# Optimization experiments

Measured on AMD Instinct MI355X. Metric: run time of the kernel, lower is better.

## Reference

```python
import jax, jax.numpy as jnp
import numpy as np

B, S, V, D = 64, 24, 50257, 300
N, E, Ln, Le = 256, 1024, 4, 4
HL = 512               # LSTM hidden size
HEADS, HD = 4, 128
OUT = HEADS * HD       # 512, GAT out dim (concat heads)
NA = 3000              # num answers


def setup_inputs() -> dict:
    key = jax.random.key(0)
    ks = jax.random.split(key, 24)
    s = 0.02
    inp = {}
    inp["question"] = jax.random.randint(ks[0], (B, S), 0, V)
    inp["question_mask"] = jnp.ones((B, S), dtype=jnp.int32)
    inp["node_tokens"] = jax.random.randint(ks[1], (B, N, Ln), 0, V)
    inp["edge_tokens"] = jax.random.randint(ks[2], (B, E, Le), 0, V)
    inp["src_ids"] = jax.random.randint(ks[3], (B, E), 0, N)
    inp["dst_ids"] = jax.random.randint(ks[4], (B, E), 0, N)
    inp["word_emb"] = jax.random.normal(ks[5], (V, D)) * s
    inp["W_ih"] = jax.random.normal(ks[6], (D, 4 * HL)) * s
    inp["W_hh"] = jax.random.normal(ks[7], (HL, 4 * HL)) * s
    inp["b_lstm"] = jnp.zeros((4 * HL,))
    inp["W_node"] = jax.random.normal(ks[8], (D, HEADS * HD)) * s
    inp["W_rel"] = jax.random.normal(ks[9], (D, HEADS * HD)) * s
    inp["a_src"] = jax.random.normal(ks[10], (HEADS, HD)) * s
    inp["a_dst"] = jax.random.normal(ks[11], (HEADS, HD)) * s
    inp["a_edge"] = jax.random.normal(ks[12], (HEADS, HD)) * s
    inp["W_edge_upd"] = jax.random.normal(ks[13], (D, D)) * s
    inp["W_qnode"] = jax.random.normal(ks[14], (HL, OUT)) * s
    inp["b_qnode"] = jnp.zeros((OUT,))
    inp["W_qedge"] = jax.random.normal(ks[15], (HL, D)) * s
    inp["b_qedge"] = jnp.zeros((D,))
    inp["W_edge_prj"] = jax.random.normal(ks[16], (D, OUT)) * s
    inp["b_edge_prj"] = jnp.zeros((OUT,))
    inp["W_mid"] = jax.random.normal(ks[17], (2 * OUT, 3 * OUT)) * s
    inp["b_mid"] = jnp.zeros((3 * OUT,))
    inp["W_pre"] = jax.random.normal(ks[18], (3 * OUT, NA)) * s
    inp["b_pre"] = jnp.zeros((NA,))
    return inp


def _lstm_last_hidden(x, mask, W_ih, W_hh, b):
    # x: [B,S,D], mask: [B,S] -> last valid hidden state [B,HL]
    h0 = jnp.zeros((x.shape[0], HL), x.dtype)
    def step(carry, t):
        h, c = carry
        xt, mt = t
        g = xt @ W_ih + h @ W_hh + b
        i, f, gg, o = jnp.split(g, 4, axis=-1)
        c_new = jax.nn.sigmoid(f) * c + jax.nn.sigmoid(i) * jnp.tanh(gg)
        h_new = jax.nn.sigmoid(o) * jnp.tanh(c_new)
        m = (mt > 0)[:, None]
        return (jnp.where(m, h_new, h), jnp.where(m, c_new, c)), None
    (h, _), _ = jax.lax.scan(step, (h0, h0), (x.transpose(1, 0, 2), mask.T))
    return h


def reference(question, question_mask, node_tokens, edge_tokens, src_ids, dst_ids,
              word_emb, W_ih, W_hh, b_lstm, W_node, W_rel, a_src, a_dst, a_edge,
              W_edge_upd, W_qnode, b_qnode, W_qedge, b_qedge, W_edge_prj, b_edge_prj,
              W_mid, b_mid, W_pre, b_pre):
    # language encoder
    seq = word_emb[question]                               # [B,S,D]
    q_emb = _lstm_last_hidden(seq, question_mask, W_ih, W_hh, b_lstm)  # [B,HL]
    # graph features: sum word embeddings of node/edge phrases (get_graph_feat)
    nf = word_emb[node_tokens].sum(2).reshape(B * N, D)    # [BN,D]
    ef = word_emb[edge_tokens].sum(2).reshape(B * E, D)    # [BE,D]
    # batched graph with global node ids
    offs = (jnp.arange(B) * N)[:, None]
    src = (src_ids + offs).reshape(-1)
    dst = (dst_ids + offs).reshape(-1)
    # multi-head GAT with edge (relation) features
    h = (nf @ W_node).reshape(B * N, HEADS, HD)
    r = (ef @ W_rel).reshape(B * E, HEADS, HD)
    logits = jax.nn.leaky_relu(
        (h[src] * a_src).sum(-1) + (h[dst] * a_dst).sum(-1) + (r * a_edge).sum(-1),
        negative_slope=0.2)                                # [BE,HEADS]
    mx = jax.ops.segment_max(logits, dst, num_segments=B * N)
    ex = jnp.exp(logits - mx[dst])
    den = jax.ops.segment_sum(ex, dst, num_segments=B * N)
    alpha = ex / (den[dst] + 1e-9)
    node_out = jax.ops.segment_sum(alpha[..., None] * (h[src] + r), dst,
                                   num_segments=B * N)
    node_out = jax.nn.elu(node_out).reshape(B, N, OUT)     # ndata['feat']
    edge_out = jax.nn.relu(ef @ W_edge_upd).reshape(B, E, D)  # edata['feat']
    # per-graph readout (dgl.unbatch + torch.sum loop == segment sum over graphs)
    nodes = node_out.sum(1)                                # [B,OUT]
    edges = edge_out.sum(1)                                # [B,D]
    # question projections + fusion
    question_edges = (q_emb @ W_qedge + b_qedge) + edges
    question_nodes = (q_emb @ W_qnode + b_qnode) + nodes
    q_edges = question_edges @ W_edge_prj + b_edge_prj
    q = jnp.concatenate([q_edges, question_nodes], axis=1)  # [B,2*OUT]
    mid = q @ W_mid + b_mid
    return mid @ W_pre + b_pre                              # [B,NA]
```

## Files before the change

### kernel.cpp

```cpp
#include <hip/hip_runtime.h>
#include <hip/hip_bf16.h>
#include <cstdint>
#include <cstddef>

typedef unsigned short u16;
typedef __attribute__((ext_vector_type(8))) short bf16x8;
typedef __attribute__((ext_vector_type(4))) float f32x4;

#define BB   64
#define SS   24
#define DD   300
#define DP   304
#define HLS  512
#define BNN  16384
#define BEE  65536
#define NAA  3000

static constexpr size_t O_COUNTS = 0;
static constexpr size_t O_FILL   = 65536;
static constexpr size_t O_ESUM   = 131072;
static constexpr size_t O_H0     = 207872;
static constexpr size_t O_C      = 338944;
static constexpr size_t Z_BYTES  = 470016;
static constexpr size_t O_H1     = 470016;
static constexpr size_t O_XPROJ  = 601088;
static constexpr size_t O_BT_NODE = O_XPROJ;
static constexpr size_t O_BT_REL  = O_XPROJ + 311296;
static constexpr size_t O_BT_EDGE = O_XPROJ + 622592;
static constexpr size_t O_NF     = 13184000;
static constexpr size_t O_EF     = 23145472;
static constexpr size_t O_HFEAT  = 62991360;
static constexpr size_t O_RFEAT  = 79768576;
static constexpr size_t O_SSRC   = 146877440;
static constexpr size_t O_SDST   = 147139584;
static constexpr size_t O_SE     = 147401728;
static constexpr size_t O_SG     = 148450304;
static constexpr size_t O_DG     = 148712448;
static constexpr size_t O_RS     = 148974592;
static constexpr size_t O_ELIST  = 149040128;
static constexpr size_t O_LG     = 149302272;
static constexpr size_t O_NOUT   = 150350848;
static constexpr size_t O_NSUM   = 167128064;
static constexpr size_t O_QN     = 167259136;
static constexpr size_t O_QE     = 167390208;
static constexpr size_t O_QCAT   = 167467008;
static constexpr size_t O_MID    = 167729152;

__device__ __forceinline__ float bf(u16 u) {
  union { unsigned int i; float f; } c; c.i = ((unsigned int)u) << 16; return c.f;
}
__device__ __forceinline__ u16 f2bu(float f) {
  union { float f; unsigned int i; } c; c.f = f;
  unsigned int r = c.i + 0x7fffu + ((c.i >> 16) & 1u);
  return (u16)(r >> 16);
}

__global__ __launch_bounds__(256) void k_zero(float* __restrict__ p, int n) {
  int i = blockIdx.x * 256 + threadIdx.x, st = gridDim.x * 256;
  for (; i < n; i += st) p[i] = 0.f;
}

__global__ __launch_bounds__(256) void k_binit(const float* __restrict__ bias,
    const float* __restrict__ extra, float* __restrict__ out, int N, int ldo, int lde) {
  int col = blockIdx.x * 256 + threadIdx.x;
  int b = blockIdx.y;
  if (col < N) {
    float v = bias ? bias[col] : 0.f;
    if (extra) v += extra[(size_t)b * lde + col];
    out[(size_t)b * ldo + col] = v;
  }
}

__global__ __launch_bounds__(256) void k_feat(const int* __restrict__ toks, const float* __restrict__ emb,
                                              u16* __restrict__ outp) {
  int tid = threadIdx.x;
  int r = blockIdx.x * 4 + (tid >> 6);
  int lane = tid & 63;
  int t0 = toks[r * 4 + 0], t1 = toks[r * 4 + 1], t2 = toks[r * 4 + 2], t3 = toks[r * 4 + 3];
  const float* e0 = emb + (size_t)t0 * DD;
  const float* e1 = emb + (size_t)t1 * DD;
  const float* e2 = emb + (size_t)t2 * DD;
  const float* e3 = emb + (size_t)t3 * DD;
#pragma unroll
  for (int p = 0; p < 2; ++p) {
    int c = p * 256 + lane * 4;
    if (c >= DP) continue;
    ushort4 o;
    if (c + 3 < DD) {
      float4 a = *(const float4*)&e0[c], b4 = *(const float4*)&e1[c];
      float4 d = *(const float4*)&e2[c], e = *(const float4*)&e3[c];
      o.x = f2bu(a.x + b4.x + d.x + e.x);
      o.y = f2bu(a.y + b4.y + d.y + e.y);
      o.z = f2bu(a.z + b4.z + d.z + e.z);
      o.w = f2bu(a.w + b4.w + d.w + e.w);
    } else {
      o.x = o.y = o.z = o.w = 0;
    }
    *(ushort4*)&outp[(size_t)r * DP + c] = o;
  }
}

__global__ __launch_bounds__(256) void k_trans(const float* __restrict__ W, int N, int Npad,
                                               u16* __restrict__ Wt) {
  __shared__ float t[32][33];
  int tx = threadIdx.x & 31;
  int ty = threadIdx.x >> 5;
  int c0 = blockIdx.x * 32;
  int k0 = blockIdx.y * 32;
#pragma unroll
  for (int r = 0; r < 4; ++r) {
    int k = k0 + ty + r * 8;
    int c = c0 + tx;
    t[ty + r * 8][tx] = (k < DD && c < N) ? W[(size_t)k * N + c] : 0.f;
  }
  __syncthreads();
#pragma unroll
  for (int r = 0; r < 4; ++r) {
    int c = c0 + ty + r * 8;
    int k = k0 + tx;
    if (c < Npad && k < DP) Wt[(size_t)c * DP + k] = f2bu(t[tx][ty + r * 8]);
  }
}

__global__ __launch_bounds__(256) void k_packW(const float* __restrict__ W, float* __restrict__ Wp) {
  int idx = blockIdx.x * 256 + threadIdx.x;
  int k = idx >> 9, j = idx & 511;
  float4 v;
  v.x = W[(size_t)k * 2048 + j];
  v.y = W[(size_t)k * 2048 + 512 + j];
  v.z = W[(size_t)k * 2048 + 1024 + j];
  v.w = W[(size_t)k * 2048 + 1536 + j];
  *(float4*)&Wp[(size_t)k * 2048 + j * 4] = v;
}

__global__ __launch_bounds__(256) void gemm_f32(
    const float* __restrict__ A, int lda, const int* __restrict__ rowmap,
    const float* __restrict__ W, int N, int K, float* __restrict__ Cf, int gatepack) {
  __shared__ float As[32][128];
  __shared__ float Ws[32][128];
  int tid = threadIdx.x;
  int tx = tid & 15, ty = tid >> 4;
  int row0 = blockIdx.y * 128, col0 = blockIdx.x * 128;
  float acc[8][8];
#pragma unroll
  for (int i = 0; i < 8; ++i)
#pragma unroll
    for (int j = 0; j < 8; ++j) acc[i][j] = 0.f;
  for (int k0 = 0; k0 < K; k0 += 32) {
    for (int s = tid; s < 1024; s += 256) {
      int r = s >> 3, kc = (s & 7) << 2, kk = k0 + kc;
      float4 v = {0.f, 0.f, 0.f, 0.f};
      if (kk + 3 < K) {
        int ar = row0 + r;
        if (rowmap) ar = rowmap[ar];
        v = *(const float4*)&A[(size_t)ar * lda + kk];
      } else if (kk < K) {
        int ar = row0 + r;
        if (rowmap) ar = rowmap[ar];
        v.x = A[(size_t)ar * lda + kk];
        if (kk + 1 < K) v.y = A[(size_t)ar * lda + kk + 1];
        if (kk + 2 < K) v.z = A[(size_t)ar * lda + kk + 2];
      }
      As[kc + 0][r] = v.x; As[kc + 1][r] = v.y; As[kc + 2][r] = v.z; As[kc + 3][r] = v.w;
    }
    for (int s = tid; s < 1024; s += 256) {
      int kr = s >> 5, nc = (s & 31) << 2, kk = k0 + kr, col = col0 + nc;
      float4 wv = {0.f, 0.f, 0.f, 0.f};
      if (kk < K && col + 3 < N) wv = *(const float4*)&W[(size_t)kk * N + col];
      *(float4*)&Ws[kr][nc] = wv;
    }
    __syncthreads();
#pragma unroll 8
    for (int k = 0; k < 32; ++k) {
      float a[8], b[8];
      *(float4*)&a[0] = *(float4*)&As[k][ty * 8];
      *(float4*)&a[4] = *(float4*)&As[k][ty * 8 + 4];
      *(float4*)&b[0] = *(float4*)&Ws[k][tx * 8];
      *(float4*)&b[4] = *(float4*)&Ws[k][tx * 8 + 4];
#pragma unroll
      for (int i = 0; i < 8; ++i)
#pragma unroll
        for (int j = 0; j < 8; ++j) acc[i][j] = fmaf(a[i], b[j], acc[i][j]);
    }
    __syncthreads();
  }
#pragma unroll
  for (int i = 0; i < 8; ++i) {
    int gr = row0 + ty * 8 + i;
#pragma unroll
    for (int j = 0; j < 8; ++j) {
      int gc = col0 + tx * 8 + j;
      if (gc < N) {
        size_t oi = gatepack ? ((size_t)gr * 2048 + ((gc & 511) << 2) + (gc >> 9))
                             : ((size_t)gr * N + gc);
        Cf[oi] = acc[i][j];
      }
    }
  }
}

__global__ __launch_bounds__(256) void gemm_mfma(
    const u16* __restrict__ A, const u16* __restrict__ Bt,
    u16* __restrict__ Cb, int N) {
  __shared__ __align__(16) u16 As[128][40];
  __shared__ __align__(16) u16 Bs[128][40];
  int tid = threadIdx.x;
  int wave = tid >> 6, lane = tid & 63;
  int wr = wave >> 1, wc = wave & 1;
  int row0 = blockIdx.y * 128, col0 = blockIdx.x * 128;
  f32x4 acc[4][4];
#pragma unroll
  for (int i = 0; i < 4; ++i)
#pragma unroll
    for (int j = 0; j < 4; ++j) acc[i][j] = (f32x4){0.f, 0.f, 0.f, 0.f};

  for (int k0 = 0; k0 < DP; k0 += 32) {
    for (int s = tid; s < 1024; s += 256) {
      int r = s >> 3, kc = (s & 7) << 2, kk = k0 + kc;
      ushort4 va = {0, 0, 0, 0}, vb = {0, 0, 0, 0};
      if (kk < DP) {
        va = *(const ushort4*)&A[(size_t)(row0 + r) * DP + kk];
        vb = *(const ushort4*)&Bt[(size_t)(col0 + r) * DP + kk];
      }
      *(ushort4*)&As[r][kc] = va;
      *(ushort4*)&Bs[r][kc] = vb;
    }
    __syncthreads();
    bf16x8 af[4], bfr[4];
    int kb = (lane >> 4) * 8;
    int rl = lane & 15;
#pragma unroll
    for (int i = 0; i < 4; ++i) {
      af[i]  = *(const bf16x8*)&As[wr * 64 + i * 16 + rl][kb];
      bfr[i] = *(const bf16x8*)&Bs[wc * 64 + i * 16 + rl][kb];
    }
#pragma unroll
    for (int i = 0; i < 4; ++i)
#pragma unroll
      for (int j = 0; j < 4; ++j)
        acc[i][j] = __builtin_amdgcn_mfma_f32_16x16x32_bf16(af[i], bfr[j], acc[i][j], 0, 0, 0);
    __syncthreads();
  }

  int g = lane >> 4, rl = lane & 15;
#pragma unroll
  for (int i = 0; i < 4; ++i)
#pragma unroll
    for (int j = 0; j < 4; ++j) {
      int gc = col0 + wc * 64 + j * 16 + rl;
#pragma unroll
      for (int reg = 0; reg < 4; ++reg) {
        int gr = row0 + wr * 64 + i * 16 + g * 4 + reg;
        Cb[(size_t)gr * N + gc] = f2bu(acc[i][j][reg]);
      }
    }
}

__global__ __launch_bounds__(256) void gemm_mfma2(
    const u16* __restrict__ A, const u16* __restrict__ Bt,
    u16* __restrict__ Cb, const float* __restrict__ aedge,
    float* __restrict__ se, float* __restrict__ bsum) {
  __shared__ __align__(16) u16 As[128][40];
  __shared__ __align__(16) u16 Bs[128][40];
  __shared__ float sered[2][128];
  int tid = threadIdx.x;
  int wave = tid >> 6, lane = tid & 63;
  int wr = wave >> 1, wc = wave & 1;
  int row0 = blockIdx.x * 128;
  int g = lane >> 4, rl = lane & 15;
  int kb = g * 8;

  for (int ct = 0; ct < 7; ++ct) {
    int col0 = ct * 128;
    f32x4 acc[4][4];
#pragma unroll
    for (int i = 0; i < 4; ++i)
#pragma unroll
      for (int j = 0; j < 4; ++j) acc[i][j] = (f32x4){0.f, 0.f, 0.f, 0.f};

    for (int k0 = 0; k0 < DP; k0 += 32) {
      for (int s = tid; s < 1024; s += 256) {
        int r = s >> 3, kc = (s & 7) << 2, kk = k0 + kc;
        ushort4 va = {0, 0, 0, 0}, vb = {0, 0, 0, 0};
        if (kk < DP) {
          va = *(const ushort4*)&A[(size_t)(row0 + r) * DP + kk];
          vb = *(const ushort4*)&Bt[(size_t)(col0 + r) * DP + kk];
        }
        *(ushort4*)&As[r][kc] = va;
        *(ushort4*)&Bs[r][kc] = vb;
      }
      __syncthreads();
      bf16x8 af[4], bfr[4];
#pragma unroll
      for (int i = 0; i < 4; ++i) {
        af[i]  = *(const bf16x8*)&As[wr * 64 + i * 16 + rl][kb];
        bfr[i] = *(const bf16x8*)&Bs[wc * 64 + i * 16 + rl][kb];
      }
#pragma unroll
      for (int i = 0; i < 4; ++i)
#pragma unroll
        for (int j = 0; j < 4; ++j)
          acc[i][j] = __builtin_amdgcn_mfma_f32_16x16x32_bf16(af[i], bfr[j], acc[i][j], 0, 0, 0);
      __syncthreads();
    }

    if (ct < 4) {
#pragma unroll
      for (int i = 0; i < 4; ++i)
#pragma unroll
        for (int j = 0; j < 4; ++j) {
          int gc = col0 + wc * 64 + j * 16 + rl;
#pragma unroll
          for (int reg = 0; reg < 4; ++reg) {
            int gr = row0 + wr * 64 + i * 16 + g * 4 + reg;
            Cb[(size_t)gr * 512 + gc] = f2bu(acc[i][j][reg]);
          }
        }
      float ce[4];
#pragma unroll
      for (int j = 0; j < 4; ++j) ce[j] = aedge[col0 + wc * 64 + j * 16 + rl];
      float p[4][4];
#pragma unroll
      for (int i = 0; i < 4; ++i)
#pragma unroll
        for (int reg = 0; reg < 4; ++reg) {
          float s = 0.f;
#pragma unroll
          for (int j = 0; j < 4; ++j) s += acc[i][j][reg] * ce[j];
          p[i][reg] = s;
        }
#pragma unroll
      for (int m = 1; m < 16; m <<= 1)
#pragma unroll
        for (int i = 0; i < 4; ++i)
#pragma unroll
          for (int reg = 0; reg < 4; ++reg)
            p[i][reg] += __shfl_xor(p[i][reg], m);
      if (rl == 0) {
#pragma unroll
        for (int i = 0; i < 4; ++i)
#pragma unroll
          for (int reg = 0; reg < 4; ++reg)
            sered[wc][wr * 64 + i * 16 + g * 4 + reg] = p[i][reg];
      }
      __syncthreads();
      if (tid < 128) se[(size_t)(row0 + tid) * 4 + ct] = sered[0][tid] + sered[1][tid];
      __syncthreads();
    } else {
      float* red = (float*)&As[0][0];
#pragma unroll
      for (int j = 0; j < 4; ++j) {
        float s = 0.f;
#pragma unroll
        for (int i = 0; i < 4; ++i)
#pragma unroll
          for (int reg = 0; reg < 4; ++reg) s += fmaxf(acc[i][j][reg], 0.f);
        red[(wr * 4 + g) * 128 + wc * 64 + j * 16 + rl] = s;
      }
      __syncthreads();
      if (tid < 128) {
        float s = 0.f;
#pragma unroll
        for (int y = 0; y < 8; ++y) s += red[y * 128 + tid];
        int c = col0 - 512 + tid;
        if (c < 300) atomicAdd(&bsum[(size_t)(row0 >> 10) * 300 + c], s);
      }
      __syncthreads();
    }
  }
}

__global__ __launch_bounds__(256) void gemm_small(
    const float* __restrict__ A, int lda, const float* __restrict__ W,
    int N, int K, int ldo, float* __restrict__ out) {
  __shared__ float As[64][256];
  int tid = threadIdx.x;
  int k0 = blockIdx.y * 256;
  int kt = min(256, K - k0);
  int col = blockIdx.x * 64 + (tid & 63);
  int bg = tid >> 6;
  int nseg = kt >> 2;
  for (int s = tid; s < 64 * nseg; s += 256) {
    int r = s / nseg, kq = s - r * nseg;
    *(float4*)&As[r][kq << 2] = *(const float4*)&A[(size_t)r * lda + k0 + (kq << 2)];
  }
  __syncthreads();
  float acc[16];
#pragma unroll
  for (int i = 0; i < 16; ++i) acc[i] = 0.f;
  if (col < N) {
    for (int k = 0; k < kt; k += 4) {
      float w0 = W[(size_t)(k0 + k) * N + col];
      float w1 = W[(size_t)(k0 + k + 1) * N + col];
      float w2 = W[(size_t)(k0 + k + 2) * N + col];
      float w3 = W[(size_t)(k0 + k + 3) * N + col];
#pragma unroll
      for (int bi = 0; bi < 16; ++bi) {
        float4 a4 = *(const float4*)&As[bg * 16 + bi][k];
        acc[bi] = fmaf(a4.x, w0, fmaf(a4.y, w1, fmaf(a4.z, w2, fmaf(a4.w, w3, acc[bi]))));
      }
    }
#pragma unroll
    for (int bi = 0; bi < 16; ++bi)
      atomicAdd(&out[(size_t)(bg * 16 + bi) * ldo + col], acc[bi]);
  }
}

__global__ __launch_bounds__(256) void k_lstm2(
    const float* __restrict__ Wp, const float* __restrict__ xproj,
    const float* __restrict__ bls, const int* __restrict__ qmask,
    const float* __restrict__ h_in, float* __restrict__ h_out, float* __restrict__ c, int t) {
  __shared__ float hs[4][512];
  int tid = threadIdx.x;
  int j = (blockIdx.x << 6) + (tid & 63);
  int bq = tid >> 6;
  int b = (blockIdx.y << 2) + bq;
  for (int i = tid; i < 2048; i += 256)
    hs[i >> 9][i & 511] = h_in[(size_t)((blockIdx.y << 2) + (i >> 9)) * 512 + (i & 511)];
  __syncthreads();
  float a0 = 0.f, a1 = 0.f, a2 = 0.f, a3 = 0.f;
#pragma unroll 8
  for (int k = 0; k < 512; ++k) {
    float hv = hs[bq][k];
    float4 w = *(const float4*)&Wp[(size_t)k * 2048 + j * 4];
    a0 = fmaf(hv, w.x, a0);
    a1 = fmaf(hv, w.y, a1);
    a2 = fmaf(hv, w.z, a2);
    a3 = fmaf(hv, w.w, a3);
  }
  size_t xb = ((size_t)b * SS + t) * 2048;
  float4 xp = *(const float4*)&xproj[xb + j * 4];
  float gi = a0 + xp.x + bls[j];
  float gf = a1 + xp.y + bls[512 + j];
  float gg = a2 + xp.z + bls[1024 + j];
  float go = a3 + xp.w + bls[1536 + j];
  float si = 1.f / (1.f + __expf(-gi));
  float sf = 1.f / (1.f + __expf(-gf));
  float so = 1.f / (1.f + __expf(-go));
  float tg = 2.f / (1.f + __expf(-2.f * gg)) - 1.f;
  int idx = b * 512 + j;
  float cold = c[idx];
  float cn = sf * cold + si * tg;
  float hn = so * (2.f / (1.f + __expf(-2.f * cn)) - 1.f);
  if (qmask[b * SS + t] > 0) { c[idx] = cn; h_out[idx] = hn; }
  else h_out[idx] = h_in[idx];
}

__global__ __launch_bounds__(256) void k_snode(const u16* __restrict__ hfeat,
    const float* __restrict__ a_src, const float* __restrict__ a_dst,
    float* __restrict__ ssrc, float* __restrict__ sdst) {
  __shared__ float as[4 * 132], ad[4 * 132];
  int tid = threadIdx.x;
  for (int i = tid; i < 512; i += 256) {
    int h = i >> 7, d = i & 127;
    as[h * 132 + d] = a_src[i];
    ad[h * 132 + d] = a_dst[i];
  }
  __syncthreads();
  int id = blockIdx.x * 256 + tid;
  int n = id >> 2, h = id & 3;
  const u16* hp = hfeat + (size_t)n * 512 + h * 128;
  float s1 = 0.f, s2 = 0.f;
  for (int d = 0; d < 128; d += 4) {
    ushort4 v = *(const ushort4*)&hp[d];
    float f0 = bf(v.x), f1 = bf(v.y), f2 = bf(v.z), f3 = bf(v.w);
    int o = h * 132 + d;
    s1 += f0 * as[o] + f1 * as[o + 1] + f2 * as[o + 2] + f3 * as[o + 3];
    s2 += f0 * ad[o] + f1 * ad[o + 1] + f2 * ad[o + 2] + f3 * ad[o + 3];
  }
  ssrc[id] = s1; sdst[id] = s2;
}

__global__ __launch_bounds__(256) void k_prep(const int* __restrict__ src, const int* __restrict__ dst,
    int* __restrict__ sg, int* __restrict__ dg, int* __restrict__ counts) {
  int i = blockIdx.x * 256 + threadIdx.x;
  int b = i >> 10;
  sg[i] = (b << 8) + src[i];
  int dgl = (b << 8) + dst[i];
  dg[i] = dgl;
  atomicAdd(&counts[dgl], 1);
}

__global__ __launch_bounds__(256) void k_scan(const int* __restrict__ counts, int* __restrict__ rs) {
  __shared__ int sc[256];
  int b = blockIdx.x, tid = threadIdx.x;
  int v = counts[b * 256 + tid];
  sc[tid] = v;
  __syncthreads();
  for (int off = 1; off < 256; off <<= 1) {
    int add = (tid >= off) ? sc[tid - off] : 0;
    __syncthreads();
    sc[tid] += add;
    __syncthreads();
  }
  rs[b * 256 + tid] = b * 1024 + sc[tid] - v;
}

__global__ __launch_bounds__(256) void k_scatter(const int* __restrict__ dg, const int* __restrict__ rs,
    int* __restrict__ fill, int* __restrict__ elist) {
  int i = blockIdx.x * 256 + threadIdx.x;
  int d = dg[i];
  int pos = rs[d] + atomicAdd(&fill[d], 1);
  elist[pos] = i;
}

__global__ __launch_bounds__(256) void k_logit(const int* __restrict__ sg, const int* __restrict__ dg,
    const float* __restrict__ ssrc, const float* __restrict__ sdst,
    const float* __restrict__ se, float* __restrict__ lg) {
  int i = blockIdx.x * 256 + threadIdx.x;
  int e = i >> 2, h = i & 3;
  float x = ssrc[sg[e] * 4 + h] + sdst[dg[e] * 4 + h] + se[i];
  lg[i] = x > 0.f ? x : 0.2f * x;
}

__global__ __launch_bounds__(256) void k_soft(const int* __restrict__ counts, const int* __restrict__ rs,
    const int* __restrict__ elist, float* __restrict__ lg) {
  int id = blockIdx.x * 256 + threadIdx.x;
  int n = id >> 2, h = id & 3;
  int deg = counts[n];
  if (deg == 0) return;
  int st = rs[n];
  float m = -1e30f;
  for (int i = 0; i < deg; ++i) { int e = elist[st + i]; m = fmaxf(m, lg[e * 4 + h]); }
  float s = 0.f;
  for (int i = 0; i < deg; ++i) {
    int e = elist[st + i];
    float p = __expf(lg[e * 4 + h] - m);
    lg[e * 4 + h] = p;
    s += p;
  }
  float inv = 1.f / (s + 1e-9f);
  for (int i = 0; i < deg; ++i) { int e = elist[st + i]; lg[e * 4 + h] *= inv; }
}

__global__ __launch_bounds__(256) void k_agg(const int* __restrict__ counts, const int* __restrict__ rs,
    const int* __restrict__ elist, const int* __restrict__ sg, const float* __restrict__ lg,
    const u16* __restrict__ hfeat, const u16* __restrict__ rfeat, u16* __restrict__ nout) {
  int n = blockIdx.x;
  int deg = counts[n], st = rs[n];
  int c1 = threadIdx.x, c2 = threadIdx.x + 256;
  float a1 = 0.f, a2 = 0.f;
  for (int i = 0; i < deg; ++i) {
    int e = elist[st + i];
    int s = sg[e];
    float al1 = lg[e * 4 + (c1 >> 7)], al2 = lg[e * 4 + (c2 >> 7)];
    a1 += al1 * (bf(hfeat[(size_t)s * 512 + c1]) + bf(rfeat[(size_t)e * 512 + c1]));
    a2 += al2 * (bf(hfeat[(size_t)s * 512 + c2]) + bf(rfeat[(size_t)e * 512 + c2]));
  }
  a1 = a1 > 0.f ? a1 : __expf(a1) - 1.f;
  a2 = a2 > 0.f ? a2 : __expf(a2) - 1.f;
  nout[(size_t)n * 512 + c1] = f2bu(a1);
  nout[(size_t)n * 512 + c2] = f2bu(a2);
}

__global__ __launch_bounds__(512) void k_nodesum(const u16* __restrict__ nout, float* __restrict__ nsum) {
  int b = blockIdx.x, col = threadIdx.x;
  float s = 0.f;
  for (int n = 0; n < 256; ++n) s += bf(nout[(size_t)((b << 8) + n) * 512 + col]);
  nsum[b * 512 + col] = s;
}

extern "C" void kernel_launch(void* const* d_in, const int* in_sizes, int n_in,
                              void* d_out, int out_size, void* d_ws, size_t ws_size,
                              hipStream_t stream) {
  const int*   question   = (const int*)d_in[0];
  const int*   qmask      = (const int*)d_in[1];
  const int*   node_toks  = (const int*)d_in[2];
  const int*   edge_toks  = (const int*)d_in[3];
  const int*   src_ids    = (const int*)d_in[4];
  const int*   dst_ids    = (const int*)d_in[5];
  const float* word_emb   = (const float*)d_in[6];
  const float* W_ih       = (const float*)d_in[7];
  const float* W_hh       = (const float*)d_in[8];
  const float* b_lstm     = (const float*)d_in[9];
  const float* W_node     = (const float*)d_in[10];
  const float* W_rel      = (const float*)d_in[11];
  const float* a_src      = (const float*)d_in[12];
  const float* a_dst      = (const float*)d_in[13];
  const float* a_edge     = (const float*)d_in[14];
  const float* W_edge_upd = (const float*)d_in[15];
  const float* W_qnode    = (const float*)d_in[16];
  const float* b_qnode    = (const float*)d_in[17];
  const float* W_qedge    = (const float*)d_in[18];
  const float* b_qedge    = (const float*)d_in[19];
  const float* W_edge_prj = (const float*)d_in[20];
  const float* b_edge_prj = (const float*)d_in[21];
  const float* W_mid      = (const float*)d_in[22];
  const float* b_mid      = (const float*)d_in[23];
  const float* W_pre      = (const float*)d_in[24];
  const float* b_pre      = (const float*)d_in[25];
  float* outp = (float*)d_out;

  char* ws = (char*)d_ws;
  int*   counts = (int*)(ws + O_COUNTS);
  int*   fill   = (int*)(ws + O_FILL);
  float* esum   = (float*)(ws + O_ESUM);
  float* h0     = (float*)(ws + O_H0);
  float* cst    = (float*)(ws + O_C);
  float* h1     = (float*)(ws + O_H1);
  float* xproj  = (float*)(ws + O_XPROJ);
  u16*   btn    = (u16*)(ws + O_BT_NODE);
  u16*   btr    = (u16*)(ws + O_BT_REL);
  u16*   bte    = (u16*)(ws + O_BT_EDGE);
  u16*   nf     = (u16*)(ws + O_NF);
  u16*   ef     = (u16*)(ws + O_EF);
  u16*   hfeat  = (u16*)(ws + O_HFEAT);
  u16*   rfeat  = (u16*)(ws + O_RFEAT);
  float* Wp     = (float*)(ws + O_RFEAT);
  float* ssrc   = (float*)(ws + O_SSRC);
  float* sdst   = (float*)(ws + O_SDST);
  float* se     = (float*)(ws + O_SE);
  int*   sg     = (int*)(ws + O_SG);
  int*   dg     = (int*)(ws + O_DG);
  int*   rs     = (int*)(ws + O_RS);
  int*   elist  = (int*)(ws + O_ELIST);
  float* lg     = (float*)(ws + O_LG);
  u16*   nout   = (u16*)(ws + O_NOUT);
  float* nsum   = (float*)(ws + O_NSUM);
  float* qn     = (float*)(ws + O_QN);
  float* qe     = (float*)(ws + O_QE);
  float* qcat   = (float*)(ws + O_QCAT);
  float* midb   = (float*)(ws + O_MID);

  k_zero<<<128, 256, 0, stream>>>((float*)ws, (int)(Z_BYTES / 4));
  k_feat<<<BNN / 4, 256, 0, stream>>>(node_toks, word_emb, nf);
  k_feat<<<BEE / 4, 256, 0, stream>>>(edge_toks, word_emb, ef);
  k_packW<<<1024, 256, 0, stream>>>(W_hh, Wp);
  gemm_f32<<<dim3(16, 12), 256, 0, stream>>>(word_emb, DD, question, W_ih, 2048, DD, xproj, 1);
  for (int t = 0; t < SS; ++t) {
    const float* hin = (t & 1) ? h1 : h0;
    float* hout = (t & 1) ? h0 : h1;
    k_lstm2<<<dim3(8, 16), 256, 0, stream>>>(Wp, xproj, b_lstm, qmask, hin, hout, cst, t);
  }
  k_trans<<<dim3(16, 10), 256, 0, stream>>>(W_node, 512, 512, btn);
  k_trans<<<dim3(16, 10), 256, 0, stream>>>(W_rel, 512, 512, btr);
  k_trans<<<dim3(12, 10), 256, 0, stream>>>(W_edge_upd, 300, 384, bte);
  gemm_mfma<<<dim3(4, 128), 256, 0, stream>>>(nf, btn, hfeat, 512);
  gemm_mfma2<<<512, 256, 0, stream>>>(ef, btr, rfeat, a_edge, se, esum);
  k_snode<<<256, 256, 0, stream>>>(hfeat, a_src, a_dst, ssrc, sdst);
  k_prep<<<256, 256, 0, stream>>>(src_ids, dst_ids, sg, dg, counts);
  k_scan<<<64, 256, 0, stream>>>(counts, rs);
  k_scatter<<<256, 256, 0, stream>>>(dg, rs, fill, elist);
  k_logit<<<1024, 256, 0, stream>>>(sg, dg, ssrc, sdst, se, lg);
  k_soft<<<256, 256, 0, stream>>>(counts, rs, elist, lg);
  k_agg<<<BNN, 256, 0, stream>>>(counts, rs, elist, sg, lg, hfeat, rfeat, nout);
  k_nodesum<<<64, 512, 0, stream>>>(nout, nsum);
  k_binit<<<dim3(2, 64), 256, 0, stream>>>(b_qnode, nsum, qn, 512, 512, 512);
  k_binit<<<dim3(2, 64), 256, 0, stream>>>(b_qedge, esum, qe, 300, 300, 300);
  gemm_small<<<dim3(8, 2), 256, 0, stream>>>(h0, 512, W_qnode, 512, 512, 512, qn);
  gemm_small<<<dim3(5, 2), 256, 0, stream>>>(h0, 512, W_qedge, 300, 512, 300, qe);
  k_binit<<<dim3(2, 64), 256, 0, stream>>>(b_edge_prj, nullptr, qcat, 512, 1024, 0);
  k_binit<<<dim3(2, 64), 256, 0, stream>>>(nullptr, qn, qcat + 512, 512, 1024, 512);
  gemm_small<<<dim3(8, 2), 256, 0, stream>>>(qe, 300, W_edge_prj, 512, 300, 1024, qcat);
  k_binit<<<dim3(6, 64), 256, 0, stream>>>(b_mid, nullptr, midb, 1536, 1536, 0);
  gemm_small<<<dim3(24, 4), 256, 0, stream>>>(qcat, 1024, W_mid, 1536, 1024, 1536, midb);
  k_binit<<<dim3(12, 64), 256, 0, stream>>>(b_pre, nullptr, outp, NAA, NAA, 0);
  gemm_small<<<dim3(47, 6), 256, 0, stream>>>(midb, 1536, W_pre, NAA, 1536, NAA, outp);
}
```

Measured before the change: 1.229 ms.

## Merge node and edge feature GEMMs into one kernel with fused attention scores

Replaces the separate node GEMM, edge GEMM and node attention-score kernel with one launch whose blocks handle either edge or node rows. Each block holds a whole 64-row A tile in shared memory and double-buffers the B tiles, and the node path computes the src/dst attention dot products in its epilogue. The LSTM step kernel is also relaunched with 128-thread blocks and twice as many blocks. The intent is fewer launches, no re-read of hfeat, more parallelism and overlap of loads with MFMA, at the cost of larger shared memory per block and smaller per-wave tiles.

```diff
diff --git a/kernel.cpp b/kernel.cpp
--- a/kernel.cpp
+++ b/kernel.cpp
@@ -199,105 +199,73 @@
   }
 }
 
-__global__ __launch_bounds__(256) void gemm_mfma(
-    const u16* __restrict__ A, const u16* __restrict__ Bt,
-    u16* __restrict__ Cb, int N) {
-  __shared__ __align__(16) u16 As[128][40];
-  __shared__ __align__(16) u16 Bs[128][40];
+__global__ __launch_bounds__(256) void gemm_feat(
+    const u16* __restrict__ efA, const u16* __restrict__ nfA,
+    const u16* __restrict__ btEF, const u16* __restrict__ btNF,
+    u16* __restrict__ rfeat, u16* __restrict__ hfeat,
+    const float* __restrict__ a_edge, const float* __restrict__ a_src, const float* __restrict__ a_dst,
+    float* __restrict__ se, float* __restrict__ ssrc, float* __restrict__ sdst,
+    float* __restrict__ esum) {
+  __shared__ __align__(16) u16 Aa[64][328];
+  __shared__ __align__(16) union {
+    u16 Bs[2][128][40];
+    float red[8][128];
+    float sered[2][64];
+  } S;
+
   int tid = threadIdx.x;
   int wave = tid >> 6, lane = tid & 63;
   int wr = wave >> 1, wc = wave & 1;
-  int row0 = blockIdx.y * 128, col0 = blockIdx.x * 128;
-  f32x4 acc[4][4];
-#pragma unroll
-  for (int i = 0; i < 4; ++i)
-#pragma unroll
-    for (int j = 0; j < 4; ++j) acc[i][j] = (f32x4){0.f, 0.f, 0.f, 0.f};
-
-  for (int k0 = 0; k0 < DP; k0 += 32) {
-    for (int s = tid; s < 1024; s += 256) {
-      int r = s >> 3, kc = (s & 7) << 2, kk = k0 + kc;
-      ushort4 va = {0, 0, 0, 0}, vb = {0, 0, 0, 0};
-      if (kk < DP) {
-        va = *(const ushort4*)&A[(size_t)(row0 + r) * DP + kk];
-        vb = *(const ushort4*)&Bt[(size_t)(col0 + r) * DP + kk];
-      }
-      *(ushort4*)&As[r][kc] = va;
-      *(ushort4*)&Bs[r][kc] = vb;
-    }
-    __syncthreads();
-    bf16x8 af[4], bfr[4];
-    int kb = (lane >> 4) * 8;
-    int rl = lane & 15;
-#pragma unroll
-    for (int i = 0; i < 4; ++i) {
-      af[i]  = *(const bf16x8*)&As[wr * 64 + i * 16 + rl][kb];
-      bfr[i] = *(const bf16x8*)&Bs[wc * 64 + i * 16 + rl][kb];
-    }
-#pragma unroll
-    for (int i = 0; i < 4; ++i)
-#pragma unroll
-      for (int j = 0; j < 4; ++j)
-        acc[i][j] = __builtin_amdgcn_mfma_f32_16x16x32_bf16(af[i], bfr[j], acc[i][j], 0, 0, 0);
-    __syncthreads();
-  }
-
-  int g = lane >> 4, rl = lane & 15;
-#pragma unroll
-  for (int i = 0; i < 4; ++i)
-#pragma unroll
-    for (int j = 0; j < 4; ++j) {
-      int gc = col0 + wc * 64 + j * 16 + rl;
-#pragma unroll
-      for (int reg = 0; reg < 4; ++reg) {
-        int gr = row0 + wr * 64 + i * 16 + g * 4 + reg;
-        Cb[(size_t)gr * N + gc] = f2bu(acc[i][j][reg]);
-      }
-    }
-}
-
-__global__ __launch_bounds__(256) void gemm_mfma2(
-    const u16* __restrict__ A, const u16* __restrict__ Bt,
-    u16* __restrict__ Cb, const float* __restrict__ aedge,
-    float* __restrict__ se, float* __restrict__ bsum) {
-  __shared__ __align__(16) u16 As[128][40];
-  __shared__ __align__(16) u16 Bs[128][40];
-  __shared__ float sered[2][128];
-  int tid = threadIdx.x;
-  int wave = tid >> 6, lane = tid & 63;
-  int wr = wave >> 1, wc = wave & 1;
-  int row0 = blockIdx.x * 128;
   int g = lane >> 4, rl = lane & 15;
   int kb = g * 8;
 
-  for (int ct = 0; ct < 7; ++ct) {
+  bool isEF = blockIdx.x < 1024;
+  int row0 = (isEF ? blockIdx.x : blockIdx.x - 1024) * 64;
+  const u16* A  = isEF ? efA  : nfA;
+  const u16* Bt = isEF ? btEF : btNF;
+  u16* Cb = isEF ? rfeat : hfeat;
+  const float* v1 = isEF ? a_edge : a_src;
+  const float* v2 = isEF ? nullptr : a_dst;
+  float* o1 = isEF ? se : ssrc;
+  float* o2 = isEF ? nullptr : sdst;
+  int NT = isEF ? 7 : 4;
+
+  for (int s = tid; s < 64 * 82; s += 256) {
+    int r = s / 82, c4 = (s - r * 82) * 4;
+    ushort4 v = {0, 0, 0, 0};
+    if (c4 < DP) v = *(const ushort4*)&A[(size_t)(row0 + r) * DP + c4];
+    *(ushort4*)&Aa[r][c4] = v;
+  }
+
+#define STAGE_B(bufv, k0v)                                              \
+  for (int s = tid; s < 1024; s += 256) {                               \
+    int rr = s >> 3, kc = (s & 7) << 2, kk = (k0v) + kc;                \
+    ushort4 vb = {0, 0, 0, 0};                                          \
+    if (kk < DP) vb = *(const ushort4*)&Bt[(size_t)(col0 + rr) * DP + kk]; \
+    *(ushort4*)&S.Bs[bufv][rr][kc] = vb;                                \
+  }
+
+  for (int ct = 0; ct < NT; ++ct) {
     int col0 = ct * 128;
-    f32x4 acc[4][4];
-#pragma unroll
-    for (int i = 0; i < 4; ++i)
+    f32x4 acc[2][4];
+#pragma unroll
+    for (int i = 0; i < 2; ++i)
 #pragma unroll
       for (int j = 0; j < 4; ++j) acc[i][j] = (f32x4){0.f, 0.f, 0.f, 0.f};
 
-    for (int k0 = 0; k0 < DP; k0 += 32) {
-      for (int s = tid; s < 1024; s += 256) {
-        int r = s >> 3, kc = (s & 7) << 2, kk = k0 + kc;
-        ushort4 va = {0, 0, 0, 0}, vb = {0, 0, 0, 0};
-        if (kk < DP) {
-          va = *(const ushort4*)&A[(size_t)(row0 + r) * DP + kk];
-          vb = *(const ushort4*)&Bt[(size_t)(col0 + r) * DP + kk];
-        }
-        *(ushort4*)&As[r][kc] = va;
-        *(ushort4*)&Bs[r][kc] = vb;
-      }
-      __syncthreads();
-      bf16x8 af[4], bfr[4];
-#pragma unroll
-      for (int i = 0; i < 4; ++i) {
-        af[i]  = *(const bf16x8*)&As[wr * 64 + i * 16 + rl][kb];
-        bfr[i] = *(const bf16x8*)&Bs[wc * 64 + i * 16 + rl][kb];
-      }
-#pragma unroll
-      for (int i = 0; i < 4; ++i)
+    STAGE_B(0, 0)
+    __syncthreads();
+    for (int ks = 0; ks < 10; ++ks) {
+      if (ks < 9) { STAGE_B((ks + 1) & 1, (ks + 1) * 32) }
+      int k0 = ks * 32, buf = ks & 1;
+      bf16x8 af[2], bfr[4];
+      af[0] = *(const bf16x8*)&Aa[wr * 32 + rl][k0 + kb];
+      af[1] = *(const bf16x8*)&Aa[wr * 32 + 16 + rl][k0 + kb];
+#pragma unroll
+      for (int j = 0; j < 4; ++j)
+        bfr[j] = *(const bf16x8*)&S.Bs[buf][wc * 64 + j * 16 + rl][kb];
+#pragma unroll
+      for (int i = 0; i < 2; ++i)
 #pragma unroll
         for (int j = 0; j < 4; ++j)
           acc[i][j] = __builtin_amdgcn_mfma_f32_16x16x32_bf16(af[i], bfr[j], acc[i][j], 0, 0, 0);
@@ -306,68 +274,75 @@
 
     if (ct < 4) {
 #pragma unroll
-      for (int i = 0; i < 4; ++i)
+      for (int i = 0; i < 2; ++i)
 #pragma unroll
         for (int j = 0; j < 4; ++j) {
           int gc = col0 + wc * 64 + j * 16 + rl;
 #pragma unroll
           for (int reg = 0; reg < 4; ++reg) {
-            int gr = row0 + wr * 64 + i * 16 + g * 4 + reg;
+            int gr = row0 + wr * 32 + i * 16 + g * 4 + reg;
             Cb[(size_t)gr * 512 + gc] = f2bu(acc[i][j][reg]);
           }
         }
-      float ce[4];
-#pragma unroll
-      for (int j = 0; j < 4; ++j) ce[j] = aedge[col0 + wc * 64 + j * 16 + rl];
-      float p[4][4];
-#pragma unroll
-      for (int i = 0; i < 4; ++i)
-#pragma unroll
-        for (int reg = 0; reg < 4; ++reg) {
-          float s = 0.f;
-#pragma unroll
-          for (int j = 0; j < 4; ++j) s += acc[i][j][reg] * ce[j];
-          p[i][reg] = s;
+      int npass = v2 ? 2 : 1;
+      for (int pass = 0; pass < npass; ++pass) {
+        const float* v = pass ? v2 : v1;
+        float ce[4];
+#pragma unroll
+        for (int j = 0; j < 4; ++j) ce[j] = v[col0 + wc * 64 + j * 16 + rl];
+        float p[2][4];
+#pragma unroll
+        for (int i = 0; i < 2; ++i)
+#pragma unroll
+          for (int reg = 0; reg < 4; ++reg) {
+            float s = 0.f;
+#pragma unroll
+            for (int j = 0; j < 4; ++j) s += acc[i][j][reg] * ce[j];
+            p[i][reg] = s;
+          }
+#pragma unroll
+        for (int m = 1; m < 16; m <<= 1)
+#pragma unroll
+          for (int i = 0; i < 2; ++i)
+#pragma unroll
+            for (int reg = 0; reg < 4; ++reg)
+              p[i][reg] += __shfl_xor(p[i][reg], m);
+        if (rl == 0) {
+#pragma unroll
+          for (int i = 0; i < 2; ++i)
+#pragma unroll
+            for (int reg = 0; reg < 4; ++reg)
+              S.sered[wc][wr * 32 + i * 16 + g * 4 + reg] = p[i][reg];
         }
-#pragma unroll
-      for (int m = 1; m < 16; m <<= 1)
-#pragma unroll
-        for (int i = 0; i < 4; ++i)
-#pragma unroll
-          for (int reg = 0; reg < 4; ++reg)
-            p[i][reg] += __shfl_xor(p[i][reg], m);
-      if (rl == 0) {
-#pragma unroll
-        for (int i = 0; i < 4; ++i)
-#pragma unroll
-          for (int reg = 0; reg < 4; ++reg)
-            sered[wc][wr * 64 + i * 16 + g * 4 + reg] = p[i][reg];
+        __syncthreads();
+        if (tid < 64) {
+          float* o = pass ? o2 : o1;
+          o[(size_t)(row0 + tid) * 4 + ct] = S.sered[0][tid] + S.sered[1][tid];
+        }
+        __syncthreads();
       }
-      __syncthreads();
-      if (tid < 128) se[(size_t)(row0 + tid) * 4 + ct] = sered[0][tid] + sered[1][tid];
-      __syncthreads();
     } else {
-      float* red = (float*)&As[0][0];
 #pragma unroll
       for (int j = 0; j < 4; ++j) {
         float s = 0.f;
 #pragma unroll
-        for (int i = 0; i < 4; ++i)
+        for (int i = 0; i < 2; ++i)
 #pragma unroll
           for (int reg = 0; reg < 4; ++reg) s += fmaxf(acc[i][j][reg], 0.f);
-        red[(wr * 4 + g) * 128 + wc * 64 + j * 16 + rl] = s;
+        S.red[wr * 4 + g][wc * 64 + j * 16 + rl] = s;
       }
       __syncthreads();
       if (tid < 128) {
         float s = 0.f;
 #pragma unroll
-        for (int y = 0; y < 8; ++y) s += red[y * 128 + tid];
+        for (int y = 0; y < 8; ++y) s += S.red[y][tid];
         int c = col0 - 512 + tid;
-        if (c < 300) atomicAdd(&bsum[(size_t)(row0 >> 10) * 300 + c], s);
+        if (c < 300) atomicAdd(&esum[(size_t)(row0 >> 10) * 300 + c], s);
       }
       __syncthreads();
     }
   }
+#undef STAGE_B
 }
 
 __global__ __launch_bounds__(256) void gemm_small(
@@ -406,17 +381,17 @@
   }
 }
 
-__global__ __launch_bounds__(256) void k_lstm2(
+__global__ __launch_bounds__(128) void k_lstm3(
     const float* __restrict__ Wp, const float* __restrict__ xproj,
     const float* __restrict__ bls, const int* __restrict__ qmask,
     const float* __restrict__ h_in, float* __restrict__ h_out, float* __restrict__ c, int t) {
   __shared__ float hs[4][512];
   int tid = threadIdx.x;
-  int j = (blockIdx.x << 6) + (tid & 63);
-  int bq = tid >> 6;
-  int b = (blockIdx.y << 2) + bq;
-  for (int i = tid; i < 2048; i += 256)
-    hs[i >> 9][i & 511] = h_in[(size_t)((blockIdx.y << 2) + (i >> 9)) * 512 + (i & 511)];
+  int j = blockIdx.x * 32 + (tid & 31);
+  int bq = tid >> 5;
+  int b = blockIdx.y * 4 + bq;
+  for (int i = tid; i < 2048; i += 128)
+    hs[i >> 9][i & 511] = h_in[(size_t)(blockIdx.y * 4 + (i >> 9)) * 512 + (i & 511)];
   __syncthreads();
   float a0 = 0.f, a1 = 0.f, a2 = 0.f, a3 = 0.f;
 #pragma unroll 8
@@ -444,31 +419,6 @@
   float hn = so * (2.f / (1.f + __expf(-2.f * cn)) - 1.f);
   if (qmask[b * SS + t] > 0) { c[idx] = cn; h_out[idx] = hn; }
   else h_out[idx] = h_in[idx];
-}
-
-__global__ __launch_bounds__(256) void k_snode(const u16* __restrict__ hfeat,
-    const float* __restrict__ a_src, const float* __restrict__ a_dst,
-    float* __restrict__ ssrc, float* __restrict__ sdst) {
-  __shared__ float as[4 * 132], ad[4 * 132];
-  int tid = threadIdx.x;
-  for (int i = tid; i < 512; i += 256) {
-    int h = i >> 7, d = i & 127;
-    as[h * 132 + d] = a_src[i];
-    ad[h * 132 + d] = a_dst[i];
-  }
-  __syncthreads();
-  int id = blockIdx.x * 256 + tid;
-  int n = id >> 2, h = id & 3;
-  const u16* hp = hfeat + (size_t)n * 512 + h * 128;
-  float s1 = 0.f, s2 = 0.f;
-  for (int d = 0; d < 128; d += 4) {
-    ushort4 v = *(const ushort4*)&hp[d];
-    float f0 = bf(v.x), f1 = bf(v.y), f2 = bf(v.z), f3 = bf(v.w);
-    int o = h * 132 + d;
-    s1 += f0 * as[o] + f1 * as[o + 1] + f2 * as[o + 2] + f3 * as[o + 3];
-    s2 += f0 * ad[o] + f1 * ad[o + 1] + f2 * ad[o + 2] + f3 * ad[o + 3];
-  }
-  ssrc[id] = s1; sdst[id] = s2;
 }
 
 __global__ __launch_bounds__(256) void k_prep(const int* __restrict__ src, const int* __restrict__ dst,
@@ -630,14 +580,13 @@
   for (int t = 0; t < SS; ++t) {
     const float* hin = (t & 1) ? h1 : h0;
     float* hout = (t & 1) ? h0 : h1;
-    k_lstm2<<<dim3(8, 16), 256, 0, stream>>>(Wp, xproj, b_lstm, qmask, hin, hout, cst, t);
+    k_lstm3<<<dim3(16, 16), 128, 0, stream>>>(Wp, xproj, b_lstm, qmask, hin, hout, cst, t);
   }
   k_trans<<<dim3(16, 10), 256, 0, stream>>>(W_node, 512, 512, btn);
   k_trans<<<dim3(16, 10), 256, 0, stream>>>(W_rel, 512, 512, btr);
   k_trans<<<dim3(12, 10), 256, 0, stream>>>(W_edge_upd, 300, 384, bte);
-  gemm_mfma<<<dim3(4, 128), 256, 0, stream>>>(nf, btn, hfeat, 512);
-  gemm_mfma2<<<512, 256, 0, stream>>>(ef, btr, rfeat, a_edge, se, esum);
-  k_snode<<<256, 256, 0, stream>>>(hfeat, a_src, a_dst, ssrc, sdst);
+  gemm_feat<<<1280, 256, 0, stream>>>(ef, nf, btr, btn, rfeat, hfeat,
+                                      a_edge, a_src, a_dst, se, ssrc, sdst, esum);
   k_prep<<<256, 256, 0, stream>>>(src_ids, dst_ids, sg, dg, counts);
   k_scan<<<64, 256, 0, stream>>>(counts, rs);
   k_scatter<<<256, 256, 0, stream>>>(dg, rs, fill, elist);
```

Measured after the change: 1.295 ms. +5.4%, slower.
